# Kernel optimization log

Hardware: AMD Instinct MI355X
Metric: run time of the kernel (lower is better)

The kernel has to match this reference:

```python
import jax, jax.numpy as jnp
import numpy as np

IN_F = 4096
OUT_F = 4096
GROUP = 128          # group_size
N_GROUPS = IN_F // GROUP  # 32
PACK = 8             # 32-bit word / 4-bit values


def setup_inputs() -> dict:
    key = jax.random.key(0)
    k1, k2, k3, k4, k5 = jax.random.split(key, 5)
    x = jax.random.normal(k1, (4, 2048, IN_F), dtype=jnp.float32)
    # packed int4 weights: each int32 holds 8 nibbles along the in_features dim
    q_weights = jax.random.randint(
        k2, (IN_F // PACK, OUT_F),
        jnp.iinfo(jnp.int32).min, jnp.iinfo(jnp.int32).max, dtype=jnp.int32)
    scales = jax.random.uniform(k3, (N_GROUPS, OUT_F), jnp.float32, 0.005, 0.02)
    # zeros stored in absolute (scale-premultiplied) units, GPTQ-style
    zeros = jax.random.uniform(k4, (N_GROUPS, OUT_F), jnp.float32, 0.0, 0.16)
    bias = jax.random.normal(k5, (OUT_F,), dtype=jnp.float32) * 0.01
    return {"x": x, "q_weights": q_weights, "scales": scales,
            "zeros": zeros, "bias": bias}


def _dequantize(q_weights, scales, zeros):
    # Unpack 8 nibbles per int32 word along in_features.
    shifts = (jnp.arange(PACK, dtype=jnp.int32) * 4)
    nib = (q_weights[:, None, :] >> shifts[None, :, None]) & 0xF  # (P, 8, O)
    q = nib.reshape(IN_F, OUT_F).astype(jnp.float32)              # (I, O)
    s = jnp.repeat(scales, GROUP, axis=0)                         # (I, O)
    z = jnp.repeat(zeros, GROUP, axis=0)                          # (I, O)
    return q * s - z


def reference(x, q_weights, scales, zeros, bias):
    # W[i, o] = scale[g(i), o] * q[i, o] - zero[g(i), o];  y = x @ W + bias
    W = _dequantize(q_weights, scales, zeros)
    out = jnp.einsum('bsi,io->bso', x, W)
    return out + bias[None, None, :]
```

## Files before the change

### kernel.cpp

```cpp
#include <hip/hip_runtime.h>
#include <hip/hip_bf16.h>

#define K_DIM 4096
#define N_DIM 4096
#define M_DIM 8192
#define NT 64

typedef __bf16 bf16x8 __attribute__((ext_vector_type(8)));
typedef float floatx4 __attribute__((ext_vector_type(4)));

__device__ __forceinline__ unsigned short f2bf(float f) {
    union { float f; unsigned u; } v; v.f = f;
    unsigned u = v.u;
    return (unsigned short)((u + 0x7FFFu + ((u >> 16) & 1u)) >> 16);
}

__global__ __launch_bounds__(256) void cast_x_kernel(const float* __restrict__ x,
                                                     unsigned short* __restrict__ xb) {
    const int t = blockIdx.x * 256 + threadIdx.x;
    const int base = t * 8;
    float4 f0 = *(const float4*)(x + base);
    float4 f1 = *(const float4*)(x + base + 4);
    int4 o;
    o.x = (int)f2bf(f0.x) | ((int)f2bf(f0.y) << 16);
    o.y = (int)f2bf(f0.z) | ((int)f2bf(f0.w) << 16);
    o.z = (int)f2bf(f1.x) | ((int)f2bf(f1.y) << 16);
    o.w = (int)f2bf(f1.z) | ((int)f2bf(f1.w) << 16);
    *(int4*)(xb + base) = o;
}

__global__ __launch_bounds__(256) void dequant_kernel(const int* __restrict__ qw,
                                                      const float* __restrict__ scales,
                                                      const float* __restrict__ zeros,
                                                      unsigned short* __restrict__ wt) {
    __shared__ int4 lds[128 * 8];
    const int tid = threadIdx.x;
    const int nb = (blockIdx.x & 31) * 128;
    const int kb = blockIdx.x >> 5;
    const int p0 = kb * 8;
    const int g = kb >> 1;

#pragma unroll
    for (int it = 0; it < 4; ++it) {
        const int w = tid + it * 256;
        const int p = w >> 7;
        const int n = w & 127;
        const unsigned word = (unsigned)qw[(p0 + p) * N_DIM + nb + n];
        const float s = scales[g * N_DIM + nb + n];
        const float z = zeros[g * N_DIM + nb + n];
        unsigned short h[8];
#pragma unroll
        for (int j = 0; j < 8; ++j) {
            float q = (float)((word >> (4 * j)) & 0xFu);
            h[j] = f2bf(q * s - z);
        }
        int4 o;
        o.x = (int)h[0] | ((int)h[1] << 16);
        o.y = (int)h[2] | ((int)h[3] << 16);
        o.z = (int)h[4] | ((int)h[5] << 16);
        o.w = (int)h[6] | ((int)h[7] << 16);
        lds[n * 8 + (p ^ (n & 7))] = o;
    }
    __syncthreads();

#pragma unroll
    for (int it = 0; it < 4; ++it) {
        const int r = (tid >> 3) + it * 32;
        const int oc = tid & 7;
        int4 v = lds[r * 8 + (oc ^ (r & 7))];
        *(int4*)(wt + (size_t)(nb + r) * K_DIM + kb * 64 + oc * 8) = v;
    }
}

__device__ __forceinline__ void gl_lds16(const unsigned short* g, unsigned short* l) {
    __builtin_amdgcn_global_load_lds((__attribute__((address_space(1))) void*)g,
                                     (__attribute__((address_space(3))) void*)l, 16, 0, 0);
}

__global__ __launch_bounds__(512, 2) void gemm_kernel(const unsigned short* __restrict__ A,
                                                      const unsigned short* __restrict__ B,
                                                      const float* __restrict__ bias,
                                                      float* __restrict__ C) {
    __shared__ unsigned short As[2 * 256 * 64];
    __shared__ unsigned short Bs[2 * 256 * 64];

    const int tid = threadIdx.x;
    const int lane = tid & 63;
    const int wave = tid >> 6;

    int bid = blockIdx.x;
    bid = (bid & 7) * 64 + (bid >> 3);
    const int tileM = (bid >> 4) * 256;
    const int tileN = (bid & 15) * 256;

    const int m0 = (wave >> 2) * 128;
    const int n0 = (wave & 3) * 64;
    const int frow = lane & 15;
    const int fkq = lane >> 4;
    const int sw = frow & 7;
    const int ch0 = (fkq ^ sw) << 3;
    const int ch1 = ((fkq ^ sw) ^ 4) << 3;

    const int r0 = tid >> 3;
    const int kcg = (tid & 7) ^ (r0 & 7);
    const int dst0 = tid * 8;

    const unsigned short* Abase = A + (size_t)(tileM + r0) * K_DIM + kcg * 8;
    const unsigned short* Bbase = B + (size_t)(tileN + r0) * K_DIM + kcg * 8;

#define STAGE_A(T, H, BUF) do {                                                        \
        const unsigned short* _s = Abase + (size_t)(H) * (128 * K_DIM) + (T) * 64;     \
        gl_lds16(_s, &As[((BUF) << 14) + ((H) << 13) + dst0]);                         \
        gl_lds16(_s + 64 * K_DIM, &As[((BUF) << 14) + ((H) << 13) + 4096 + dst0]);     \
    } while (0)
#define STAGE_B(T, H, BUF) do {                                                        \
        const unsigned short* _s = Bbase + (size_t)(H) * (128 * K_DIM) + (T) * 64;     \
        gl_lds16(_s, &Bs[((BUF) << 14) + ((H) << 13) + dst0]);                         \
        gl_lds16(_s + 64 * K_DIM, &Bs[((BUF) << 14) + ((H) << 13) + 4096 + dst0]);     \
    } while (0)

    floatx4 acc[8][4];
#pragma unroll
    for (int i = 0; i < 8; ++i)
#pragma unroll
        for (int j = 0; j < 4; ++j) acc[i][j] = (floatx4){0.f, 0.f, 0.f, 0.f};

    STAGE_B(0, 0, 0); STAGE_B(0, 1, 0); STAGE_A(0, 0, 0); STAGE_A(0, 1, 0);
    STAGE_B(1, 0, 1); STAGE_B(1, 1, 1); STAGE_A(1, 0, 1);
    asm volatile("s_waitcnt vmcnt(6)" ::: "memory");
    __builtin_amdgcn_s_barrier();

    bf16x8 a[4][2], b[4][2];

#pragma unroll 2
    for (int t = 0; t < NT; ++t) {
        const int buf = t & 1;
        const int bo = buf << 14;

#pragma unroll
        for (int mi = 0; mi < 4; ++mi) {
            const int row = m0 + mi * 16 + frow;
            a[mi][0] = *(const bf16x8*)&As[bo + row * 64 + ch0];
            a[mi][1] = *(const bf16x8*)&As[bo + row * 64 + ch1];
        }
#pragma unroll
        for (int ni = 0; ni < 2; ++ni) {
            const int row = n0 + ni * 16 + frow;
            b[ni][0] = *(const bf16x8*)&Bs[bo + row * 64 + ch0];
            b[ni][1] = *(const bf16x8*)&Bs[bo + row * 64 + ch1];
        }
        if (t + 1 < NT) STAGE_A(t + 1, 1, buf ^ 1);
        __builtin_amdgcn_s_setprio(1);
#pragma unroll
        for (int mi = 0; mi < 4; ++mi)
#pragma unroll
            for (int ni = 0; ni < 2; ++ni)
#pragma unroll
                for (int kh = 0; kh < 2; ++kh)
                    acc[mi][ni] = __builtin_amdgcn_mfma_f32_16x16x32_bf16(
                        a[mi][kh], b[ni][kh], acc[mi][ni], 0, 0, 0);
        __builtin_amdgcn_s_setprio(0);
        __builtin_amdgcn_s_barrier();

#pragma unroll
        for (int ni = 2; ni < 4; ++ni) {
            const int row = n0 + ni * 16 + frow;
            b[ni][0] = *(const bf16x8*)&Bs[bo + row * 64 + ch0];
            b[ni][1] = *(const bf16x8*)&Bs[bo + row * 64 + ch1];
        }
        if (t + 2 < NT) STAGE_B(t + 2, 0, buf);
        __builtin_amdgcn_s_setprio(1);
#pragma unroll
        for (int mi = 0; mi < 4; ++mi)
#pragma unroll
            for (int ni = 2; ni < 4; ++ni)
#pragma unroll
                for (int kh = 0; kh < 2; ++kh)
                    acc[mi][ni] = __builtin_amdgcn_mfma_f32_16x16x32_bf16(
                        a[mi][kh], b[ni][kh], acc[mi][ni], 0, 0, 0);
        __builtin_amdgcn_s_setprio(0);
        __builtin_amdgcn_s_barrier();

#pragma unroll
        for (int mi = 0; mi < 4; ++mi) {
            const int row = m0 + 64 + mi * 16 + frow;
            a[mi][0] = *(const bf16x8*)&As[bo + row * 64 + ch0];
            a[mi][1] = *(const bf16x8*)&As[bo + row * 64 + ch1];
        }
        if (t + 2 < NT) STAGE_B(t + 2, 1, buf);
        __builtin_amdgcn_s_setprio(1);
#pragma unroll
        for (int mi = 0; mi < 4; ++mi)
#pragma unroll
            for (int ni = 2; ni < 4; ++ni)
#pragma unroll
                for (int kh = 0; kh < 2; ++kh)
                    acc[4 + mi][ni] = __builtin_amdgcn_mfma_f32_16x16x32_bf16(
                        a[mi][kh], b[ni][kh], acc[4 + mi][ni], 0, 0, 0);
        __builtin_amdgcn_s_setprio(0);
        __builtin_amdgcn_s_barrier();

        if (t + 2 < NT) STAGE_A(t + 2, 0, buf);
        __builtin_amdgcn_s_setprio(1);
#pragma unroll
        for (int mi = 0; mi < 4; ++mi)
#pragma unroll
            for (int ni = 0; ni < 2; ++ni)
#pragma unroll
                for (int kh = 0; kh < 2; ++kh)
                    acc[4 + mi][ni] = __builtin_amdgcn_mfma_f32_16x16x32_bf16(
                        a[mi][kh], b[ni][kh], acc[4 + mi][ni], 0, 0, 0);
        __builtin_amdgcn_s_setprio(0);
        if (t + 2 < NT) { asm volatile("s_waitcnt vmcnt(6)" ::: "memory"); }
        else            { asm volatile("s_waitcnt vmcnt(0)" ::: "memory"); }
        __builtin_amdgcn_s_barrier();
    }
#undef STAGE_A
#undef STAGE_B

    asm volatile("s_waitcnt vmcnt(0)" ::: "memory");

    const int crow = (lane >> 4) * 4;
    const int ccol = lane & 15;
#pragma unroll
    for (int ni = 0; ni < 4; ++ni) {
        const int gcol = tileN + n0 + ni * 16 + ccol;
        const float bv = bias[gcol];
#pragma unroll
        for (int mi = 0; mi < 8; ++mi) {
            const int rbase = (tileM + m0 + mi * 16 + crow) * N_DIM + gcol;
#pragma unroll
            for (int r = 0; r < 4; ++r)
                C[rbase + r * N_DIM] = acc[mi][ni][r] + bv;
        }
    }
}

extern "C" void kernel_launch(void* const* d_in, const int* in_sizes, int n_in,
                              void* d_out, int out_size, void* d_ws, size_t ws_size,
                              hipStream_t stream) {
    (void)in_sizes; (void)n_in; (void)out_size; (void)ws_size;
    const float* x      = (const float*)d_in[0];
    const int*   qw     = (const int*)d_in[1];
    const float* scales = (const float*)d_in[2];
    const float* zeros  = (const float*)d_in[3];
    const float* bias   = (const float*)d_in[4];
    float* out = (float*)d_out;

    unsigned short* xb = (unsigned short*)d_ws;
    unsigned short* wt = xb + (size_t)M_DIM * K_DIM;

    hipLaunchKernelGGL(cast_x_kernel, dim3(16384), dim3(256), 0, stream, x, xb);
    hipLaunchKernelGGL(dequant_kernel, dim3(2048), dim3(256), 0, stream, qw, scales, zeros, wt);
    hipLaunchKernelGGL(gemm_kernel, dim3(512), dim3(512), 0, stream, xb, wt, bias, out);
}
```

Before: 462.1 us.

## Restructure GEMM main loop to single barrier per k-tile with register prefetch

Replaces the four-phase interleaved schedule (four barriers per k-tile, staged loads two tiles ahead) with one that issues all next-tile global-to-LDS loads at the start, runs all 32 MFMAs in one block, then waits and prefetches the next tile's low A/B fragments into registers after a single barrier. This is meant to cut barrier overhead and keep the MFMA sequence uninterrupted. In exchange, the prefetch distance drops to one tile with a full vmcnt(0) wait each iteration, so global latency may be exposed, and register pressure rises from holding separate low and high fragment sets.

```diff
diff --git a/kernel.cpp b/kernel.cpp
--- a/kernel.cpp
+++ b/kernel.cpp
@@ -125,100 +125,105 @@
 #pragma unroll
         for (int j = 0; j < 4; ++j) acc[i][j] = (floatx4){0.f, 0.f, 0.f, 0.f};
 
+    bf16x8 aL[4][2], aH[4][2], bL[2][2], bH[2][2];
+
     STAGE_B(0, 0, 0); STAGE_B(0, 1, 0); STAGE_A(0, 0, 0); STAGE_A(0, 1, 0);
-    STAGE_B(1, 0, 1); STAGE_B(1, 1, 1); STAGE_A(1, 0, 1);
-    asm volatile("s_waitcnt vmcnt(6)" ::: "memory");
+    asm volatile("s_waitcnt vmcnt(0)" ::: "memory");
     __builtin_amdgcn_s_barrier();
-
-    bf16x8 a[4][2], b[4][2];
+    asm volatile("" ::: "memory");
+#pragma unroll
+    for (int mi = 0; mi < 4; ++mi) {
+        const int row = m0 + mi * 16 + frow;
+        aL[mi][0] = *(const bf16x8*)&As[row * 64 + ch0];
+        aL[mi][1] = *(const bf16x8*)&As[row * 64 + ch1];
+    }
+#pragma unroll
+    for (int ni = 0; ni < 2; ++ni) {
+        const int row = n0 + ni * 16 + frow;
+        bL[ni][0] = *(const bf16x8*)&Bs[row * 64 + ch0];
+        bL[ni][1] = *(const bf16x8*)&Bs[row * 64 + ch1];
+    }
 
 #pragma unroll 2
     for (int t = 0; t < NT; ++t) {
         const int buf = t & 1;
         const int bo = buf << 14;
-
-#pragma unroll
-        for (int mi = 0; mi < 4; ++mi) {
-            const int row = m0 + mi * 16 + frow;
-            a[mi][0] = *(const bf16x8*)&As[bo + row * 64 + ch0];
-            a[mi][1] = *(const bf16x8*)&As[bo + row * 64 + ch1];
-        }
+        const int obo = bo ^ 16384;
+
+        if (t + 1 < NT) {
+            STAGE_B(t + 1, 0, buf ^ 1); STAGE_B(t + 1, 1, buf ^ 1);
+            STAGE_A(t + 1, 0, buf ^ 1); STAGE_A(t + 1, 1, buf ^ 1);
+        }
+
 #pragma unroll
         for (int ni = 0; ni < 2; ++ni) {
-            const int row = n0 + ni * 16 + frow;
-            b[ni][0] = *(const bf16x8*)&Bs[bo + row * 64 + ch0];
-            b[ni][1] = *(const bf16x8*)&Bs[bo + row * 64 + ch1];
-        }
-        if (t + 1 < NT) STAGE_A(t + 1, 1, buf ^ 1);
-        __builtin_amdgcn_s_setprio(1);
-#pragma unroll
-        for (int mi = 0; mi < 4; ++mi)
-#pragma unroll
-            for (int ni = 0; ni < 2; ++ni)
-#pragma unroll
-                for (int kh = 0; kh < 2; ++kh)
-                    acc[mi][ni] = __builtin_amdgcn_mfma_f32_16x16x32_bf16(
-                        a[mi][kh], b[ni][kh], acc[mi][ni], 0, 0, 0);
-        __builtin_amdgcn_s_setprio(0);
-        __builtin_amdgcn_s_barrier();
-
-#pragma unroll
-        for (int ni = 2; ni < 4; ++ni) {
-            const int row = n0 + ni * 16 + frow;
-            b[ni][0] = *(const bf16x8*)&Bs[bo + row * 64 + ch0];
-            b[ni][1] = *(const bf16x8*)&Bs[bo + row * 64 + ch1];
-        }
-        if (t + 2 < NT) STAGE_B(t + 2, 0, buf);
-        __builtin_amdgcn_s_setprio(1);
-#pragma unroll
-        for (int mi = 0; mi < 4; ++mi)
-#pragma unroll
-            for (int ni = 2; ni < 4; ++ni)
-#pragma unroll
-                for (int kh = 0; kh < 2; ++kh)
-                    acc[mi][ni] = __builtin_amdgcn_mfma_f32_16x16x32_bf16(
-                        a[mi][kh], b[ni][kh], acc[mi][ni], 0, 0, 0);
-        __builtin_amdgcn_s_setprio(0);
-        __builtin_amdgcn_s_barrier();
-
+            const int row = n0 + (ni + 2) * 16 + frow;
+            bH[ni][0] = *(const bf16x8*)&Bs[bo + row * 64 + ch0];
+            bH[ni][1] = *(const bf16x8*)&Bs[bo + row * 64 + ch1];
+        }
 #pragma unroll
         for (int mi = 0; mi < 4; ++mi) {
             const int row = m0 + 64 + mi * 16 + frow;
-            a[mi][0] = *(const bf16x8*)&As[bo + row * 64 + ch0];
-            a[mi][1] = *(const bf16x8*)&As[bo + row * 64 + ch1];
-        }
-        if (t + 2 < NT) STAGE_B(t + 2, 1, buf);
+            aH[mi][0] = *(const bf16x8*)&As[bo + row * 64 + ch0];
+            aH[mi][1] = *(const bf16x8*)&As[bo + row * 64 + ch1];
+        }
+
         __builtin_amdgcn_s_setprio(1);
 #pragma unroll
         for (int mi = 0; mi < 4; ++mi)
 #pragma unroll
-            for (int ni = 2; ni < 4; ++ni)
+            for (int ni = 0; ni < 2; ++ni)
+#pragma unroll
+                for (int kh = 0; kh < 2; ++kh)
+                    acc[mi][ni] = __builtin_amdgcn_mfma_f32_16x16x32_bf16(
+                        aL[mi][kh], bL[ni][kh], acc[mi][ni], 0, 0, 0);
+#pragma unroll
+        for (int mi = 0; mi < 4; ++mi)
+#pragma unroll
+            for (int ni = 0; ni < 2; ++ni)
+#pragma unroll
+                for (int kh = 0; kh < 2; ++kh)
+                    acc[mi][2 + ni] = __builtin_amdgcn_mfma_f32_16x16x32_bf16(
+                        aL[mi][kh], bH[ni][kh], acc[mi][2 + ni], 0, 0, 0);
+#pragma unroll
+        for (int mi = 0; mi < 4; ++mi)
+#pragma unroll
+            for (int ni = 0; ni < 2; ++ni)
 #pragma unroll
                 for (int kh = 0; kh < 2; ++kh)
                     acc[4 + mi][ni] = __builtin_amdgcn_mfma_f32_16x16x32_bf16(
-                        a[mi][kh], b[ni][kh], acc[4 + mi][ni], 0, 0, 0);
+                        aH[mi][kh], bL[ni][kh], acc[4 + mi][ni], 0, 0, 0);
+#pragma unroll
+        for (int mi = 0; mi < 4; ++mi)
+#pragma unroll
+            for (int ni = 0; ni < 2; ++ni)
+#pragma unroll
+                for (int kh = 0; kh < 2; ++kh)
+                    acc[4 + mi][2 + ni] = __builtin_amdgcn_mfma_f32_16x16x32_bf16(
+                        aH[mi][kh], bH[ni][kh], acc[4 + mi][2 + ni], 0, 0, 0);
         __builtin_amdgcn_s_setprio(0);
+
+        asm volatile("s_waitcnt vmcnt(0)" ::: "memory");
         __builtin_amdgcn_s_barrier();
-
-        if (t + 2 < NT) STAGE_A(t + 2, 0, buf);
-        __builtin_amdgcn_s_setprio(1);
-#pragma unroll
-        for (int mi = 0; mi < 4; ++mi)
-#pragma unroll
-            for (int ni = 0; ni < 2; ++ni)
-#pragma unroll
-                for (int kh = 0; kh < 2; ++kh)
-                    acc[4 + mi][ni] = __builtin_amdgcn_mfma_f32_16x16x32_bf16(
-                        a[mi][kh], b[ni][kh], acc[4 + mi][ni], 0, 0, 0);
-        __builtin_amdgcn_s_setprio(0);
-        if (t + 2 < NT) { asm volatile("s_waitcnt vmcnt(6)" ::: "memory"); }
-        else            { asm volatile("s_waitcnt vmcnt(0)" ::: "memory"); }
-        __builtin_amdgcn_s_barrier();
+        asm volatile("" ::: "memory");
+
+        if (t + 1 < NT) {
+#pragma unroll
+            for (int mi = 0; mi < 4; ++mi) {
+                const int row = m0 + mi * 16 + frow;
+                aL[mi][0] = *(const bf16x8*)&As[obo + row * 64 + ch0];
+                aL[mi][1] = *(const bf16x8*)&As[obo + row * 64 + ch1];
+            }
+#pragma unroll
+            for (int ni = 0; ni < 2; ++ni) {
+                const int row = n0 + ni * 16 + frow;
+                bL[ni][0] = *(const bf16x8*)&Bs[obo + row * 64 + ch0];
+                bL[ni][1] = *(const bf16x8*)&Bs[obo + row * 64 + ch1];
+            }
+        }
     }
 #undef STAGE_A
 #undef STAGE_B
-
-    asm volatile("s_waitcnt vmcnt(0)" ::: "memory");
 
     const int crow = (lane >> 4) * 4;
     const int ccol = lane & 15;
```

After: 498.7 us. +7.9%, slower.
